# Performance work log

Measured on AMD Instinct MI355X. Metric: run time of the kernel, lower is better.

The kernel has to match this reference:

```python
import jax, jax.numpy as jnp
import numpy as np


def setup_inputs() -> dict:
    key = jax.random.key(0)
    k1, k2, k3, k4 = jax.random.split(key, 4)
    B, T, I, H = 64, 512, 256, 512
    stdv = 1.0 / np.sqrt(H)
    x = jax.random.normal(k1, (B, T, I), dtype=jnp.float32)
    weight_ih = jax.random.uniform(k2, (I, 4 * H), dtype=jnp.float32, minval=-stdv, maxval=stdv)
    weight_hh = jax.random.uniform(k3, (H, 4 * H), dtype=jnp.float32, minval=-stdv, maxval=stdv)
    bias_ih = jax.random.uniform(k4, (4 * H,), dtype=jnp.float32, minval=-stdv, maxval=stdv)
    return {"x": x, "weight_ih": weight_ih, "weight_hh": weight_hh, "bias_ih": bias_ih}


def reference(x, weight_ih, weight_hh, bias_ih):
    B, T, I = x.shape
    H = weight_hh.shape[0]
    # Precompute input projections for all timesteps: [T, B, 4H]
    x_proj = jnp.einsum('bti,ig->tbg', x, weight_ih) + bias_ih

    def step(carry, xp):
        h, c = carry
        gates = xp + h @ weight_hh  # [B, 4H]
        ig, fg, cg, og = jnp.split(gates, 4, axis=1)
        ig = jax.nn.sigmoid(ig)
        fg = jax.nn.sigmoid(fg)
        cg = jnp.tanh(cg)
        # NOTE: original code applies NO sigmoid to outgate and adds it:
        # hy = outgate * tanh(cy) + outgate
        cy = fg * c + ig * cg
        hy = og * jnp.tanh(cy) + og
        return (hy, cy), hy

    h0 = jnp.zeros((B, H), dtype=x.dtype)
    c0 = jnp.zeros((B, H), dtype=x.dtype)
    _, hs = jax.lax.scan(step, (h0, c0), x_proj)  # hs: [T, B, H]
    return jnp.transpose(hs, (1, 0, 2))  # [B, T, H]
```

## Files before the change

kernel.cpp:

```cpp
#include <hip/hip_runtime.h>
#include <hip/hip_bf16.h>
#include <math.h>

#define BB 64
#define TT 512
#define II 256
#define HH 512
#define GG 2048
#define NBLK 128
#define KP  520
#define XPAD 264

typedef unsigned char u8;
typedef unsigned short u16;
typedef unsigned int u32;
typedef __attribute__((ext_vector_type(4))) int   i32x4;
typedef __attribute__((ext_vector_type(2))) int   i32x2;
typedef __attribute__((ext_vector_type(8))) short short8v;
typedef __attribute__((ext_vector_type(4))) float f32x4;

__device__ __forceinline__ u16 f2bf(float f) {
    unsigned u = __float_as_uint(f);
    unsigned r = (u + 0x7fff + ((u >> 16) & 1)) >> 16;
    return (u16)r;
}
__device__ __forceinline__ float bf2f(u16 h) {
    return __uint_as_float(((unsigned)h) << 16);
}
__device__ __forceinline__ float sigf(float v) {
    return 1.f / (1.f + __expf(-v));
}
__device__ __forceinline__ float tanh_s(float v) {
    float a = fabsf(v);
    float e = __expf(2.f * a);
    float r = 1.f - 2.f / (e + 1.f);
    return copysignf(r, v);
}

#define HLD(dst, base, OFF) \
    asm volatile("global_load_dwordx4 %0, %1, off offset:" OFF " sc0 sc1" \
                 : "=v"(dst) : "v"(base))
#define XLD(dst, voff, sbase) \
    asm volatile("global_load_dwordx4 %0, %1, %2" \
                 : "=v"(dst) : "v"(voff), "s"(sbase))
#define CVTPK(d, lo, hi) \
    asm("v_cvt_pk_bf16_f32 %0, %1, %2" : "=v"(d) : "v"(lo), "v"(hi))

__global__ void __launch_bounds__(64, 1) slstm_kernel(
    const float* __restrict__ x, const float* __restrict__ wih,
    const float* __restrict__ whh, const float* __restrict__ bias,
    float* __restrict__ out, u8* __restrict__ flagb,
    u16* __restrict__ hbuf )
{
    __shared__ u16 lds_whh[4 * 16 * KP];
    __shared__ u16 lds_wih[64 * XPAD];
    __shared__ u16 lds_x[16 * XPAD];

    const int l  = threadIdx.x;
    const int bt = blockIdx.x & 3;
    const int js = blockIdx.x >> 2;
    const int b0 = bt * 16, j0 = js * 16;
    const int c  = l & 15, kq = l >> 4;

    for (int q = 0; q < 4; ++q)
        for (int kk = 0; kk < 128; ++kk) {
            int k = kk * 4 + kq;
            lds_whh[(q * 16 + c) * KP + k] =
                f2bf(whh[(size_t)k * GG + q * 512 + j0 + c]);
        }
    for (int q = 0; q < 4; ++q)
        for (int kk = 0; kk < 64; ++kk) {
            int k = kk * 4 + kq;
            lds_wih[(q * 16 + c) * XPAD + k] =
                f2bf(wih[(size_t)k * GG + q * 512 + j0 + c]);
        }

    float bq[4];
#pragma unroll
    for (int q = 0; q < 4; ++q) bq[q] = bias[q * 512 + j0 + c];

    float cst[4] = {0.f, 0.f, 0.f, 0.f};
    __syncthreads();

    const u32 vbase = (u32)(b0 * TT * II * 4) + 16 * (u32)l;

    f32x4 xr[16];
#pragma unroll
    for (int r = 0; r < 16; ++r) {
        u32 vo = vbase + (u32)(r * TT * II * 4);
        XLD(xr[r], vo, x);
    }
    asm volatile("s_waitcnt vmcnt(0)" ::: "memory");
    __builtin_amdgcn_sched_barrier(0);
#pragma unroll
    for (int r = 0; r < 16; ++r) {
        i32x2 p;
        CVTPK(p[0], xr[r][0], xr[r][1]);
        CVTPK(p[1], xr[r][2], xr[r][3]);
        *(i32x2*)&lds_x[r * XPAD + 4 * l] = p;
    }

    for (int t = 0; t < TT; ++t) {
        i32x4 w0, w1;
        const u8* fb = flagb;
        if (t > 0) {
            fb = flagb + ((size_t)(bt * TT + (t - 1))) * 32;
            asm volatile(
                "global_load_dwordx4 %0, %2, off sc0 sc1\n\t"
                "global_load_dwordx4 %1, %2, off offset:16 sc0 sc1"
                : "=v"(w0), "=v"(w1) : "v"(fb) : "memory");
        }

        const int tn = (t + 1 < TT) ? t + 1 : TT - 1;
#pragma unroll
        for (int r = 0; r < 16; ++r) {
            u32 vo = vbase + (u32)(r * TT * II * 4) + (u32)(tn * II * 4);
            XLD(xr[r], vo, x);
        }

        f32x4 acc[4];
#pragma unroll
        for (int q = 0; q < 4; ++q) acc[q] = (f32x4){bq[q], bq[q], bq[q], bq[q]};
#pragma unroll
        for (int s = 0; s < 8; ++s) {
            short8v a = *(const short8v*)&lds_x[c * XPAD + 32 * s + 8 * kq];
#pragma unroll
            for (int q = 0; q < 4; ++q) {
                short8v b = *(const short8v*)&lds_wih[(q * 16 + c) * XPAD + 32 * s + 8 * kq];
                acc[q] = __builtin_amdgcn_mfma_f32_16x16x32_bf16(a, b, acc[q], 0, 0, 0);
            }
        }

        if (t > 0) {
            asm volatile("s_waitcnt vmcnt(16)" ::: "memory");
            __builtin_amdgcn_sched_barrier(0);
            int m = w0[0] & w0[1] & w0[2] & w0[3] & w1[0] & w1[1] & w1[2] & w1[3];
            while (m != 0x01010101) {
                asm volatile(
                    "global_load_dwordx4 %0, %2, off sc0 sc1\n\t"
                    "global_load_dwordx4 %1, %2, off offset:16 sc0 sc1\n\t"
                    "s_waitcnt vmcnt(0)"
                    : "=v"(w0), "=v"(w1) : "v"(fb) : "memory");
                m = w0[0] & w0[1] & w0[2] & w0[3] & w1[0] & w1[1] & w1[2] & w1[3];
            }
            __builtin_amdgcn_sched_barrier(0);
        }

        const int rp = (t - 1) & 1;
        const u16* hb = hbuf + (size_t)(rp * 2) * BB * HH + (size_t)(b0 + c) * HH + 8 * kq;
        const u16* lb = hb + BB * HH;
        i32x4 h0,h1,h2,h3,h4,h5,h6,h7,h8,h9,h10,h11,h12,h13,h14,h15;
        i32x4 g0,g1,g2,g3,g4,g5,g6,g7,g8,g9,g10,g11,g12,g13,g14,g15;
        HLD(h0, hb,   "0"); HLD(g0, lb,   "0");
        HLD(h1, hb,  "64"); HLD(g1, lb,  "64");
        HLD(h2, hb, "128"); HLD(g2, lb, "128");
        HLD(h3, hb, "192"); HLD(g3, lb, "192");
        HLD(h4, hb, "256"); HLD(g4, lb, "256");
        HLD(h5, hb, "320"); HLD(g5, lb, "320");
        HLD(h6, hb, "384"); HLD(g6, lb, "384");
        HLD(h7, hb, "448"); HLD(g7, lb, "448");
        HLD(h8, hb, "512"); HLD(g8, lb, "512");
        HLD(h9, hb, "576"); HLD(g9, lb, "576");
        HLD(h10,hb, "640"); HLD(g10,lb, "640");
        HLD(h11,hb, "704"); HLD(g11,lb, "704");
        HLD(h12,hb, "768"); HLD(g12,lb, "768");
        HLD(h13,hb, "832"); HLD(g13,lb, "832");
        HLD(h14,hb, "896"); HLD(g14,lb, "896");
        HLD(h15,hb, "960"); HLD(g15,lb, "960");

#define HMM(S, FH, FL) do {                                                     \
        short8v ah_ = __builtin_bit_cast(short8v, FH);                          \
        short8v al_ = __builtin_bit_cast(short8v, FL);                          \
        _Pragma("unroll")                                                       \
        for (int q = 0; q < 4; ++q) {                                           \
            short8v b_ = *(const short8v*)&lds_whh[(q * 16 + c) * KP + 32 * (S) + 8 * kq]; \
            acc[q] = __builtin_amdgcn_mfma_f32_16x16x32_bf16(ah_, b_, acc[q], 0, 0, 0); \
            acc[q] = __builtin_amdgcn_mfma_f32_16x16x32_bf16(al_, b_, acc[q], 0, 0, 0); \
        }                                                                       \
    } while (0)

        asm volatile("s_waitcnt vmcnt(16)" ::: "memory");
        __builtin_amdgcn_sched_barrier(0);
        HMM(0, h0, g0); HMM(1, h1, g1); HMM(2, h2, g2); HMM(3, h3, g3);
        HMM(4, h4, g4); HMM(5, h5, g5); HMM(6, h6, g6); HMM(7, h7, g7);
        asm volatile("s_waitcnt vmcnt(0)" ::: "memory");
        __builtin_amdgcn_sched_barrier(0);
        HMM(8, h8, g8); HMM(9, h9, g9); HMM(10,h10,g10); HMM(11,h11,g11);
        HMM(12,h12,g12); HMM(13,h13,g13); HMM(14,h14,g14); HMM(15,h15,g15);

        const int wp = t & 1;
        u16* hdst_hi = hbuf + (size_t)(wp * 2) * BB * HH;
        u16* hdst_lo = hdst_hi + BB * HH;
        const int j = j0 + c;
#pragma unroll
        for (int rg = 0; rg < 4; ++rg) {
            int b = b0 + kq * 4 + rg;
            float ig = sigf(acc[0][rg]);
            float fg = sigf(acc[1][rg]);
            float cg = tanh_s(acc[2][rg]);
            float og = acc[3][rg];
            float cy = fg * cst[rg] + ig * cg;
            cst[rg] = cy;
            float hy = og * tanh_s(cy) + og;
            out[((size_t)b * TT + t) * HH + j] = hy;
            u16 hi = f2bf(hy);
            float lo = hy - bf2f(hi);
            __hip_atomic_store(&hdst_hi[(size_t)b * HH + j], hi,
                               __ATOMIC_RELAXED, __HIP_MEMORY_SCOPE_AGENT);
            __hip_atomic_store(&hdst_lo[(size_t)b * HH + j], f2bf(lo),
                               __ATOMIC_RELAXED, __HIP_MEMORY_SCOPE_AGENT);
        }

#pragma unroll
        for (int r = 0; r < 16; ++r) {
            i32x2 p;
            CVTPK(p[0], xr[r][0], xr[r][1]);
            CVTPK(p[1], xr[r][2], xr[r][3]);
            *(i32x2*)&lds_x[r * XPAD + 4 * l] = p;
        }

        asm volatile("s_waitcnt vmcnt(0)" ::: "memory");
        if (l == 0)
            __hip_atomic_store(flagb + ((size_t)(bt * TT + t)) * 32 + js, (u8)1,
                               __ATOMIC_RELAXED, __HIP_MEMORY_SCOPE_AGENT);
    }
}

extern "C" void kernel_launch(void* const* d_in, const int* in_sizes, int n_in,
                              void* d_out, int out_size, void* d_ws, size_t ws_size,
                              hipStream_t stream) {
    const float* x    = (const float*)d_in[0];
    const float* wih  = (const float*)d_in[1];
    const float* whh  = (const float*)d_in[2];
    const float* bias = (const float*)d_in[3];
    float* out = (float*)d_out;

    u8*  flagb = (u8*)d_ws;
    u16* hbuf  = (u16*)((char*)d_ws + 65536);
    size_t clear = 65536 + (size_t)2 * 2 * BB * HH * sizeof(u16);
    hipMemsetAsync(d_ws, 0, clear, stream);

    hipLaunchKernelGGL(slstm_kernel, dim3(NBLK), dim3(64), 0, stream,
                       x, wih, whh, bias, out, flagb, hbuf);
}
```

Before: 2.546 ms.

## Interleave hi/lo bf16 hidden state into packed u32 and overlap x-projection with h loads

The hidden-state exchange buffer changes from separate hi and lo bf16 planes to one interleaved u32 array, so each element is written with a single atomic swap instead of two stores. Readers unpack the pairs with byte permutes. Half of the x-projection MFMAs are moved after the h loads are issued, to hide global load latency on the recurrent critical path. The flag store becomes an inline-asm byte store with sc0 sc1. This adds permute ALU work per step and relies on the chosen cache bits for cross-block visibility.

```diff
diff --git a/kernel.cpp b/kernel.cpp
--- a/kernel.cpp
+++ b/kernel.cpp
@@ -46,11 +46,13 @@
 #define CVTPK(d, lo, hi) \
     asm("v_cvt_pk_bf16_f32 %0, %1, %2" : "=v"(d) : "v"(lo), "v"(hi))
 
+#define PERM __builtin_amdgcn_perm
+
 __global__ void __launch_bounds__(64, 1) slstm_kernel(
     const float* __restrict__ x, const float* __restrict__ wih,
     const float* __restrict__ whh, const float* __restrict__ bias,
     float* __restrict__ out, u8* __restrict__ flagb,
-    u16* __restrict__ hbuf )
+    u32* __restrict__ hbuf )
 {
     __shared__ u16 lds_whh[4 * 16 * KP];
     __shared__ u16 lds_wih[64 * XPAD];
@@ -99,6 +101,35 @@
         CVTPK(p[1], xr[r][2], xr[r][3]);
         *(i32x2*)&lds_x[r * XPAD + 4 * l] = p;
     }
+
+#define XPS(S) do {                                                             \
+        short8v a = *(const short8v*)&lds_x[c * XPAD + 32 * (S) + 8 * kq];      \
+        _Pragma("unroll")                                                       \
+        for (int q = 0; q < 4; ++q) {                                           \
+            short8v b = *(const short8v*)&lds_wih[(q * 16 + c) * XPAD + 32 * (S) + 8 * kq]; \
+            acc[q] = __builtin_amdgcn_mfma_f32_16x16x32_bf16(a, b, acc[q], 0, 0, 0); \
+        }                                                                       \
+    } while (0)
+
+#define HMM(S, U, V) do {                                                       \
+        i32x4 ahw, alw;                                                         \
+        ahw[0] = (int)PERM((u32)(U)[1], (u32)(U)[0], 0x05040100u);              \
+        ahw[1] = (int)PERM((u32)(U)[3], (u32)(U)[2], 0x05040100u);              \
+        ahw[2] = (int)PERM((u32)(V)[1], (u32)(V)[0], 0x05040100u);              \
+        ahw[3] = (int)PERM((u32)(V)[3], (u32)(V)[2], 0x05040100u);              \
+        alw[0] = (int)PERM((u32)(U)[1], (u32)(U)[0], 0x07060302u);              \
+        alw[1] = (int)PERM((u32)(U)[3], (u32)(U)[2], 0x07060302u);              \
+        alw[2] = (int)PERM((u32)(V)[1], (u32)(V)[0], 0x07060302u);              \
+        alw[3] = (int)PERM((u32)(V)[3], (u32)(V)[2], 0x07060302u);              \
+        short8v ah_ = __builtin_bit_cast(short8v, ahw);                         \
+        short8v al_ = __builtin_bit_cast(short8v, alw);                         \
+        _Pragma("unroll")                                                       \
+        for (int q = 0; q < 4; ++q) {                                           \
+            short8v b_ = *(const short8v*)&lds_whh[(q * 16 + c) * KP + 32 * (S) + 8 * kq]; \
+            acc[q] = __builtin_amdgcn_mfma_f32_16x16x32_bf16(ah_, b_, acc[q], 0, 0, 0); \
+            acc[q] = __builtin_amdgcn_mfma_f32_16x16x32_bf16(al_, b_, acc[q], 0, 0, 0); \
+        }                                                                       \
+    } while (0)
 
     for (int t = 0; t < TT; ++t) {
         i32x4 w0, w1;
@@ -121,15 +152,7 @@
         f32x4 acc[4];
 #pragma unroll
         for (int q = 0; q < 4; ++q) acc[q] = (f32x4){bq[q], bq[q], bq[q], bq[q]};
-#pragma unroll
-        for (int s = 0; s < 8; ++s) {
-            short8v a = *(const short8v*)&lds_x[c * XPAD + 32 * s + 8 * kq];
-#pragma unroll
-            for (int q = 0; q < 4; ++q) {
-                short8v b = *(const short8v*)&lds_wih[(q * 16 + c) * XPAD + 32 * s + 8 * kq];
-                acc[q] = __builtin_amdgcn_mfma_f32_16x16x32_bf16(a, b, acc[q], 0, 0, 0);
-            }
-        }
+        XPS(0); XPS(1); XPS(2); XPS(3);
 
         if (t > 0) {
             asm volatile("s_waitcnt vmcnt(16)" ::: "memory");
@@ -147,50 +170,40 @@
         }
 
         const int rp = (t - 1) & 1;
-        const u16* hb = hbuf + (size_t)(rp * 2) * BB * HH + (size_t)(b0 + c) * HH + 8 * kq;
-        const u16* lb = hb + BB * HH;
-        i32x4 h0,h1,h2,h3,h4,h5,h6,h7,h8,h9,h10,h11,h12,h13,h14,h15;
-        i32x4 g0,g1,g2,g3,g4,g5,g6,g7,g8,g9,g10,g11,g12,g13,g14,g15;
-        HLD(h0, hb,   "0"); HLD(g0, lb,   "0");
-        HLD(h1, hb,  "64"); HLD(g1, lb,  "64");
-        HLD(h2, hb, "128"); HLD(g2, lb, "128");
-        HLD(h3, hb, "192"); HLD(g3, lb, "192");
-        HLD(h4, hb, "256"); HLD(g4, lb, "256");
-        HLD(h5, hb, "320"); HLD(g5, lb, "320");
-        HLD(h6, hb, "384"); HLD(g6, lb, "384");
-        HLD(h7, hb, "448"); HLD(g7, lb, "448");
-        HLD(h8, hb, "512"); HLD(g8, lb, "512");
-        HLD(h9, hb, "576"); HLD(g9, lb, "576");
-        HLD(h10,hb, "640"); HLD(g10,lb, "640");
-        HLD(h11,hb, "704"); HLD(g11,lb, "704");
-        HLD(h12,hb, "768"); HLD(g12,lb, "768");
-        HLD(h13,hb, "832"); HLD(g13,lb, "832");
-        HLD(h14,hb, "896"); HLD(g14,lb, "896");
-        HLD(h15,hb, "960"); HLD(g15,lb, "960");
-
-#define HMM(S, FH, FL) do {                                                     \
-        short8v ah_ = __builtin_bit_cast(short8v, FH);                          \
-        short8v al_ = __builtin_bit_cast(short8v, FL);                          \
-        _Pragma("unroll")                                                       \
-        for (int q = 0; q < 4; ++q) {                                           \
-            short8v b_ = *(const short8v*)&lds_whh[(q * 16 + c) * KP + 32 * (S) + 8 * kq]; \
-            acc[q] = __builtin_amdgcn_mfma_f32_16x16x32_bf16(ah_, b_, acc[q], 0, 0, 0); \
-            acc[q] = __builtin_amdgcn_mfma_f32_16x16x32_bf16(al_, b_, acc[q], 0, 0, 0); \
-        }                                                                       \
-    } while (0)
+        const u32* hb = hbuf + (size_t)rp * BB * HH + (size_t)(b0 + c) * HH + 8 * kq;
+        i32x4 y0,y1,y2,y3,y4,y5,y6,y7,y8,y9,y10,y11,y12,y13,y14,y15;
+        i32x4 z0,z1,z2,z3,z4,z5,z6,z7,z8,z9,z10,z11,z12,z13,z14,z15;
+        HLD(y0, hb,    "0"); HLD(z0, hb,   "16");
+        HLD(y1, hb,  "128"); HLD(z1, hb,  "144");
+        HLD(y2, hb,  "256"); HLD(z2, hb,  "272");
+        HLD(y3, hb,  "384"); HLD(z3, hb,  "400");
+        HLD(y4, hb,  "512"); HLD(z4, hb,  "528");
+        HLD(y5, hb,  "640"); HLD(z5, hb,  "656");
+        HLD(y6, hb,  "768"); HLD(z6, hb,  "784");
+        HLD(y7, hb,  "896"); HLD(z7, hb,  "912");
+        HLD(y8, hb, "1024"); HLD(z8, hb, "1040");
+        HLD(y9, hb, "1152"); HLD(z9, hb, "1168");
+        HLD(y10,hb, "1280"); HLD(z10,hb, "1296");
+        HLD(y11,hb, "1408"); HLD(z11,hb, "1424");
+        HLD(y12,hb, "1536"); HLD(z12,hb, "1552");
+        HLD(y13,hb, "1664"); HLD(z13,hb, "1680");
+        HLD(y14,hb, "1792"); HLD(z14,hb, "1808");
+        HLD(y15,hb, "1920"); HLD(z15,hb, "1936");
+
+        XPS(4); XPS(5); XPS(6); XPS(7);
+        __builtin_amdgcn_sched_barrier(0);
 
         asm volatile("s_waitcnt vmcnt(16)" ::: "memory");
         __builtin_amdgcn_sched_barrier(0);
-        HMM(0, h0, g0); HMM(1, h1, g1); HMM(2, h2, g2); HMM(3, h3, g3);
-        HMM(4, h4, g4); HMM(5, h5, g5); HMM(6, h6, g6); HMM(7, h7, g7);
+        HMM(0, y0, z0); HMM(1, y1, z1); HMM(2, y2, z2); HMM(3, y3, z3);
+        HMM(4, y4, z4); HMM(5, y5, z5); HMM(6, y6, z6); HMM(7, y7, z7);
         asm volatile("s_waitcnt vmcnt(0)" ::: "memory");
         __builtin_amdgcn_sched_barrier(0);
-        HMM(8, h8, g8); HMM(9, h9, g9); HMM(10,h10,g10); HMM(11,h11,g11);
-        HMM(12,h12,g12); HMM(13,h13,g13); HMM(14,h14,g14); HMM(15,h15,g15);
+        HMM(8, y8, z8); HMM(9, y9, z9); HMM(10,y10,z10); HMM(11,y11,z11);
+        HMM(12,y12,z12); HMM(13,y13,z13); HMM(14,y14,z14); HMM(15,y15,z15);
 
         const int wp = t & 1;
-        u16* hdst_hi = hbuf + (size_t)(wp * 2) * BB * HH;
-        u16* hdst_lo = hdst_hi + BB * HH;
+        u32* hdst = hbuf + (size_t)wp * BB * HH;
         const int j = j0 + c;
 #pragma unroll
         for (int rg = 0; rg < 4; ++rg) {
@@ -205,10 +218,10 @@
             out[((size_t)b * TT + t) * HH + j] = hy;
             u16 hi = f2bf(hy);
             float lo = hy - bf2f(hi);
-            __hip_atomic_store(&hdst_hi[(size_t)b * HH + j], hi,
-                               __ATOMIC_RELAXED, __HIP_MEMORY_SCOPE_AGENT);
-            __hip_atomic_store(&hdst_lo[(size_t)b * HH + j], f2bf(lo),
-                               __ATOMIC_RELAXED, __HIP_MEMORY_SCOPE_AGENT);
+            u32 pk = (u32)hi | ((u32)f2bf(lo) << 16);
+            u32* ap = hdst + (size_t)b * HH + j;
+            asm volatile("global_atomic_swap %0, %1, off sc1"
+                         :: "v"(ap), "v"(pk) : "memory");
         }
 
 #pragma unroll
@@ -220,9 +233,12 @@
         }
 
         asm volatile("s_waitcnt vmcnt(0)" ::: "memory");
-        if (l == 0)
-            __hip_atomic_store(flagb + ((size_t)(bt * TT + t)) * 32 + js, (u8)1,
-                               __ATOMIC_RELAXED, __HIP_MEMORY_SCOPE_AGENT);
+        if (l == 0) {
+            u8* fa = flagb + ((size_t)(bt * TT + t)) * 32 + js;
+            u32 one = 1u;
+            asm volatile("global_store_byte %0, %1, off sc0 sc1"
+                         :: "v"(fa), "v"(one) : "memory");
+        }
     }
 }
 
@@ -236,9 +252,9 @@
     float* out = (float*)d_out;
 
     u8*  flagb = (u8*)d_ws;
-    u16* hbuf  = (u16*)((char*)d_ws + 65536);
-    size_t clear = 65536 + (size_t)2 * 2 * BB * HH * sizeof(u16);
-    hipMemsetAsync(d_ws, 0, clear, stream);
+    u32* hbuf  = (u32*)((char*)d_ws + 65536);
+    size_t clear = 65536 + (size_t)2 * BB * HH * sizeof(u32);
+    (void)hipMemsetAsync(d_ws, 0, clear, stream);
 
     hipLaunchKernelGGL(slstm_kernel, dim3(NBLK), dim3(64), 0, stream,
                        x, wih, whh, bias, out, flagb, hbuf);
```

After: 2.595 ms. No clear change (+2.0%).
